# Performance work log

Hardware: AMD Instinct MI355X
Metric: run time of the kernel (lower is better)

The kernel has to match this reference:

```python
import jax, jax.numpy as jnp
import numpy as np

FEAT = 1433
HID = 2
NUM_CLASS = 7
EPS = 1e-5  # torch BatchNorm1d default eps


def _bn_softsign(h, gamma, beta):
    # BatchNorm1d in training mode: batch stats over (batch, length) per channel.
    mu = h.mean(axis=(0, 2), keepdims=True)
    var = h.var(axis=(0, 2), keepdims=True)  # biased, matches torch normalization
    hn = (h - mu) * jax.lax.rsqrt(var + EPS)
    hn = hn * gamma[None, :, None] + beta[None, :, None]
    return hn / (1.0 + jnp.abs(hn))  # Softsign


def feature_adjacency(x, y):
    # (x.unsqueeze(-1) * y.unsqueeze(-2)).sum(dim=1) with x channel dim == 1
    # reduces to an outer product of x[:,0] with neighbor.sum over K.
    adj = jnp.einsum('bf,bg->bfg', x.sum(1), y.sum(1))  # [B,F,F]
    adj = adj + jnp.swapaxes(adj, -1, -2)
    adj = jnp.sqrt(adj)
    # row_normalize: divide by sum over dim 1, zero out inf/nan
    norm = adj / adj.sum(axis=1, keepdims=True)
    norm = jnp.where(jnp.isfinite(norm), norm, 0.0)
    return norm + jnp.eye(FEAT, dtype=x.dtype)


def featbrd(x, adj, W, b):
    # adjacency-based feature conv: y[b,c,f] = sum_g adj[(b),f,g] x[b,c,g],
    # then 1x1 conv over channels (Conv1d kernel_size=1).
    if adj.shape[0] == 1:
        y = jnp.einsum('fg,bcg->bcf', adj[0], x)
    else:
        y = jnp.einsum('bfg,bcg->bcf', adj, x)
    return jnp.einsum('oc,bcf->bof', W, y) + b[None, :, None]


def setup_inputs() -> dict:
    key = jax.random.key(0)
    ks = jax.random.split(key, 10)
    B, K = 64, 8
    inp = {
        'x': jax.random.uniform(ks[0], (B, 1, FEAT), dtype=jnp.float32),
        'neighbor': jax.random.uniform(ks[1], (B, K, FEAT), dtype=jnp.float32),
        'adj_buf': jnp.zeros((1, FEAT, FEAT), jnp.float32),
        'W1': jax.random.normal(ks[2], (HID, 1), jnp.float32) * 0.5,
        'b1': jnp.zeros((HID,), jnp.float32),
        'W2': jax.random.normal(ks[3], (HID, HID), jnp.float32) * 0.5,
        'b2': jnp.zeros((HID,), jnp.float32),
        'g1': jnp.ones((HID,), jnp.float32),
        'be1': jnp.zeros((HID,), jnp.float32),
        'g2': jnp.ones((HID,), jnp.float32),
        'be2': jnp.zeros((HID,), jnp.float32),
        'Wc': jax.random.normal(ks[4], (NUM_CLASS, FEAT * HID), jnp.float32) * 0.02,
        'bc': jnp.zeros((NUM_CLASS,), jnp.float32),
    }
    return inp


def reference(x, neighbor, adj_buf, W1, b1, W2, b2, g1, be1, g2, be2, Wc, bc):
    fadj = feature_adjacency(x, neighbor)          # [B,F,F]
    adj_tot = adj_buf + fadj.sum(0)                # [1,F,F] (buffer starts at zero)
    h = _bn_softsign(featbrd(x, fadj, W1, b1), g1, be1)      # [B,HID,F]
    h = _bn_softsign(featbrd(h, adj_tot, W2, b2), g2, be2)   # [B,HID,F]
    flat = h.reshape(h.shape[0], -1)               # Flatten (C then F, row-major)
    return flat @ Wc.T + bc
```

## Files before the change

### kernel.cpp

```cpp
#include <hip/hip_runtime.h>
#include <hip/hip_bf16.h>
#include <math.h>

constexpr int F   = 1433;
constexpr int NB  = 64;
constexpr int KN  = 8;
constexpr int BF  = NB * F;
constexpr float EPS = 1e-5f;

constexpr int SF  = 16;
constexpr int CH  = (F + SF - 1) / SF;
constexpr int AbS = 1440;
constexpr int SK  = 15;
constexpr int KCH = 96;
constexpr int FT  = 16;
constexpr int NAB = 540;
constexpr int NST = 256;

constexpr int O_YS  = 0;
constexpr int O_DP  = O_YS + BF;
constexpr int O_Y1P = O_DP + SF * BF;
constexpr int O_P   = O_Y1P + SF * BF;
constexpr int O_Y1  = O_P + 4 * BF;
constexpr int O_Y2  = O_Y1 + BF;
constexpr int O_G2P = O_Y2 + 2 * BF;
constexpr int O_AB  = O_G2P + SK * 128 * F;
constexpr int O_ST  = O_AB + (F * AbS) / 2;

__global__ __launch_bounds__(256) void k_D(const float* __restrict__ x,
                                           const float* __restrict__ nbr,
                                           float* __restrict__ DP,
                                           float* __restrict__ ys_out) {
  __shared__ __align__(16) float2 xy[F];
  const int b = blockIdx.x, s = blockIdx.y;
  for (int i = threadIdx.x; i < F; i += 256) {
    const float* p = nbr + (size_t)b * KN * F + i;
    float acc = 0.f;
#pragma unroll
    for (int k = 0; k < KN; ++k) acc += p[k * F];
    xy[i] = make_float2(x[b * F + i], acc);
  }
  __syncthreads();
  if (s == 0) {
    for (int i = threadIdx.x; i < F; i += 256) ys_out[b * F + i] = xy[i].y;
  }
  const int cs = s * CH, cn = min(CH, F - cs);
  float gx[6], gy[6], acc[6] = {};
#pragma unroll
  for (int j = 0; j < 6; ++j) {
    int g = threadIdx.x + 256 * j;
    float2 p = (g < F) ? xy[g] : make_float2(0.f, 0.f);
    gx[j] = p.x; gy[j] = p.y;
  }
#pragma unroll 8
  for (int i = 0; i < cn; ++i) {
    float2 p = xy[cs + i];
#pragma unroll
    for (int j = 0; j < 6; ++j)
      acc[j] += __builtin_amdgcn_sqrtf(fmaf(gy[j], p.x, gx[j] * p.y));
  }
#pragma unroll
  for (int j = 0; j < 6; ++j) {
    int g = threadIdx.x + 256 * j;
    if (g < F) DP[(size_t)s * BF + b * F + g] = acc[j];
  }
}

__global__ __launch_bounds__(256) void k_y1(const float* __restrict__ x,
                                            const float* __restrict__ ys,
                                            const float* __restrict__ DP,
                                            float* __restrict__ Y1P,
                                            float4* __restrict__ P) {
  __shared__ __align__(16) float4 pl[CH];
  const int b = blockIdx.x, s = blockIdx.y;
  const int cs = s * CH, cn = min(CH, F - cs);
  for (int i = threadIdx.x; i < cn; i += 256) {
    int g = cs + i;
    float d = 0.f;
#pragma unroll
    for (int t = 0; t < SF; ++t) d += DP[(size_t)t * BF + b * F + g];
    float inv = (d > 0.f) ? 1.f / d : 0.f;
    float xv = x[b * F + g], yv = ys[b * F + g];
    float4 pv = make_float4(xv, yv, xv * inv, inv);
    pl[i] = pv;
    P[b * F + g] = pv;
  }
  __syncthreads();
  float fx[6], fy[6], acc[6] = {};
#pragma unroll
  for (int j = 0; j < 6; ++j) {
    int f = threadIdx.x + 256 * j;
    fx[j] = (f < F) ? x[b * F + f] : 0.f;
    fy[j] = (f < F) ? ys[b * F + f] : 0.f;
  }
#pragma unroll 8
  for (int i = 0; i < cn; ++i) {
    float4 p = pl[i];
#pragma unroll
    for (int j = 0; j < 6; ++j)
      acc[j] = fmaf(__builtin_amdgcn_sqrtf(fmaf(fx[j], p.y, fy[j] * p.x)), p.z, acc[j]);
  }
#pragma unroll
  for (int j = 0; j < 6; ++j) {
    int f = threadIdx.x + 256 * j;
    if (f < F) Y1P[(size_t)s * BF + b * F + f] = acc[j];
  }
}

__global__ __launch_bounds__(256) void k_Astats(const float* __restrict__ x,
                                                const float* __restrict__ ys,
                                                const float4* __restrict__ P,
                                                const float* __restrict__ Y1P,
                                                __hip_bfloat16* __restrict__ Ab,
                                                float* __restrict__ y1,
                                                float* __restrict__ st) {
  const int bid = blockIdx.x;
  if (bid < NAB) {
    __shared__ float2 fxy[FT][NB];
    const int gx = bid % 6, fy = bid / 6;
    const int fbase = fy * FT;
    for (int i = threadIdx.x; i < FT * NB; i += 256) {
      int b = i >> 4, j = i & 15;
      int f = fbase + j;
      float vx = 0.f, vy = 0.f;
      if (f < F) { vx = x[b * F + f]; vy = ys[b * F + f]; }
      fxy[j][b] = make_float2(vx, vy);
    }
    __syncthreads();
    const int g = gx * 256 + threadIdx.x;
    if (g >= AbS) return;
    if (g < F) {
      float acc[FT] = {};
#pragma unroll 2
      for (int b = 0; b < NB; ++b) {
        float4 p = P[b * F + g];
#pragma unroll
        for (int j = 0; j < FT; ++j) {
          float2 w = fxy[j][b];
          acc[j] = fmaf(__builtin_amdgcn_sqrtf(fmaf(w.x, p.y, p.x * w.y)), p.w, acc[j]);
        }
      }
#pragma unroll
      for (int j = 0; j < FT; ++j) {
        int f = fbase + j;
        if (f < F) Ab[(size_t)f * AbS + g] = __float2bfloat16(acc[j]);
      }
    } else {
#pragma unroll
      for (int j = 0; j < FT; ++j) {
        int f = fbase + j;
        if (f < F) Ab[(size_t)f * AbS + g] = __float2bfloat16(0.f);
      }
    }
  } else {
    const int sid = bid - NAB;
    float s = 0.f, sq = 0.f;
    for (int i = sid * 256 + threadIdx.x; i < BF; i += NST * 256) {
      float v = x[i];
#pragma unroll
      for (int k = 0; k < SF; ++k) v += Y1P[(size_t)k * BF + i];
      y1[i] = v;
      s += v; sq += v * v;
    }
#pragma unroll
    for (int o = 32; o; o >>= 1) {
      s += __shfl_down(s, o, 64);
      sq += __shfl_down(sq, o, 64);
    }
    __shared__ float ls[4], lq[4];
    int wave = threadIdx.x >> 6, lane = threadIdx.x & 63;
    if (lane == 0) { ls[wave] = s; lq[wave] = sq; }
    __syncthreads();
    if (threadIdx.x == 0) {
      atomicAdd(&st[0], ls[0] + ls[1] + ls[2] + ls[3]);
      atomicAdd(&st[1], lq[0] + lq[1] + lq[2] + lq[3]);
    }
  }
}

__global__ __launch_bounds__(256) void k_gemm(const ushort* __restrict__ Ab,
                                              const float* __restrict__ y1,
                                              const float* __restrict__ st,
                                              const float* __restrict__ W1,
                                              const float* __restrict__ g1,
                                              const float* __restrict__ be1,
                                              float* __restrict__ G2P) {
  const float mu = st[0] / (float)BF;
  const float var = st[1] / (float)BF - mu * mu;
  const float wa = W1[0], wb = W1[1];
  const float k0 = wa * g1[0] / sqrtf(wa * wa * var + EPS);
  const float k1 = wb * g1[1] / sqrtf(wb * wb * var + EPS);
  const float c0 = -k0 * mu + be1[0];
  const float c1 = -k1 * mu + be1[1];

  __shared__ __align__(16) float Al[32 * 36];
  __shared__ __align__(16) float Hl[32 * 132];
  const int f0 = blockIdx.x * 32;
  const int gs = blockIdx.y * KCH;
  const int tid = threadIdx.x;
  const int ffs = tid >> 3;
  const int g4s = (tid & 7) * 4;
  const int hb = tid & 7;
  const int hg = tid >> 3;
  const int fsub = (tid & 7) * 4;
  const int msub = (tid >> 3) * 4;
  float acc[4][4] = {};

  for (int c = 0; c < 3; ++c) {
    const int gb = gs + c * 32;
    {
      const int f = f0 + ffs;
      uint2 av = make_uint2(0u, 0u);
      if (f < F) av = *(const uint2*)&Ab[(size_t)f * AbS + gb + g4s];
      Al[(g4s + 0) * 36 + ffs] = __uint_as_float(av.x << 16);
      Al[(g4s + 1) * 36 + ffs] = __uint_as_float(av.x & 0xffff0000u);
      Al[(g4s + 2) * 36 + ffs] = __uint_as_float(av.y << 16);
      Al[(g4s + 3) * 36 + ffs] = __uint_as_float(av.y & 0xffff0000u);
    }
#pragma unroll
    for (int r = 0; r < 8; ++r) {
      const int b = hb + 8 * r;
      const int gl = min(gb + hg, F - 1);
      const float v = y1[b * F + gl];
      float h0 = fmaf(k0, v, c0); h0 = h0 / (1.f + fabsf(h0));
      float h1 = fmaf(k1, v, c1); h1 = h1 / (1.f + fabsf(h1));
      *(float2*)&Hl[hg * 132 + 2 * b] = make_float2(h0, h1);
    }
    __syncthreads();
#pragma unroll 4
    for (int gi = 0; gi < 32; ++gi) {
      float4 a4 = *(const float4*)&Al[gi * 36 + fsub];
      float4 h4 = *(const float4*)&Hl[gi * 132 + msub];
      float av[4] = {a4.x, a4.y, a4.z, a4.w};
      float hv[4] = {h4.x, h4.y, h4.z, h4.w};
#pragma unroll
      for (int i = 0; i < 4; ++i)
#pragma unroll
        for (int j = 0; j < 4; ++j)
          acc[i][j] = fmaf(av[i], hv[j], acc[i][j]);
    }
    __syncthreads();
  }

  float* dst = G2P + (size_t)blockIdx.y * 128 * F;
#pragma unroll
  for (int i = 0; i < 4; ++i) {
    int f = f0 + fsub + i;
    if (f < F) {
#pragma unroll
      for (int j = 0; j < 4; ++j)
        dst[(msub + j) * F + f] = acc[i][j];
    }
  }
}

__global__ __launch_bounds__(256) void k_stats2(const float* __restrict__ y1,
                                                const float* __restrict__ G2P,
                                                const float* __restrict__ st,
                                                const float* __restrict__ W1,
                                                const float* __restrict__ g1,
                                                const float* __restrict__ be1,
                                                float* __restrict__ y2,
                                                float* __restrict__ stw) {
  const float mu = st[0] / (float)BF;
  const float var = st[1] / (float)BF - mu * mu;
  const float wa = W1[0], wb = W1[1];
  const float k0 = wa * g1[0] / sqrtf(wa * wa * var + EPS);
  const float k1 = wb * g1[1] / sqrtf(wb * wb * var + EPS);
  const float c0 = -k0 * mu + be1[0];
  const float c1 = -k1 * mu + be1[1];

  float su = 0.f, sv = 0.f, suu = 0.f, svv = 0.f, suv = 0.f;
  for (int i = blockIdx.x * 256 + threadIdx.x; i < BF; i += gridDim.x * 256) {
    int b = i / F, f = i - b * F;
    float w = y1[i];
    float h0 = fmaf(k0, w, c0); h0 = h0 / (1.f + fabsf(h0));
    float h1 = fmaf(k1, w, c1); h1 = h1 / (1.f + fabsf(h1));
    int iu = (2 * b) * F + f, iv = iu + F;
    float u = 64.f * h0, v = 64.f * h1;
#pragma unroll
    for (int s = 0; s < SK; ++s) {
      u += G2P[(size_t)s * 128 * F + iu];
      v += G2P[(size_t)s * 128 * F + iv];
    }
    y2[iu] = u; y2[iv] = v;
    su += u; sv += v; suu += u * u; svv += v * v; suv += u * v;
  }
#pragma unroll
  for (int o = 32; o; o >>= 1) {
    su += __shfl_down(su, o, 64);
    sv += __shfl_down(sv, o, 64);
    suu += __shfl_down(suu, o, 64);
    svv += __shfl_down(svv, o, 64);
    suv += __shfl_down(suv, o, 64);
  }
  __shared__ float red[5][4];
  int wave = threadIdx.x >> 6, lane = threadIdx.x & 63;
  if (lane == 0) {
    red[0][wave] = su; red[1][wave] = sv; red[2][wave] = suu;
    red[3][wave] = svv; red[4][wave] = suv;
  }
  __syncthreads();
  if (threadIdx.x == 0) {
    atomicAdd(&stw[2], red[0][0] + red[0][1] + red[0][2] + red[0][3]);
    atomicAdd(&stw[3], red[1][0] + red[1][1] + red[1][2] + red[1][3]);
    atomicAdd(&stw[4], red[2][0] + red[2][1] + red[2][2] + red[2][3]);
    atomicAdd(&stw[5], red[3][0] + red[3][1] + red[3][2] + red[3][3]);
    atomicAdd(&stw[6], red[4][0] + red[4][1] + red[4][2] + red[4][3]);
  }
}

__global__ __launch_bounds__(256) void k_out(const float* __restrict__ y2,
                                             const float* __restrict__ st,
                                             const float* __restrict__ W2,
                                             const float* __restrict__ b2,
                                             const float* __restrict__ g2,
                                             const float* __restrict__ be2,
                                             const float* __restrict__ Wc,
                                             const float* __restrict__ bc,
                                             float* __restrict__ out) {
  float n = (float)BF;
  float Eu = st[2] / n, Ev = st[3] / n;
  float Euu = st[4] / n, Evv = st[5] / n, Euv = st[6] / n;
  float cA[2], cB[2], cC[2];
#pragma unroll
  for (int o = 0; o < 2; ++o) {
    float w0 = W2[o * 2 + 0], w1 = W2[o * 2 + 1];
    float mean = w0 * Eu + w1 * Ev + b2[o];
    float Eh2 = w0 * w0 * Euu + 2.f * w0 * w1 * Euv + w1 * w1 * Evv +
                2.f * b2[o] * (w0 * Eu + w1 * Ev) + b2[o] * b2[o];
    float var = Eh2 - mean * mean;
    float inv = g2[o] / sqrtf(var + EPS);
    cA[o] = w0 * inv;
    cB[o] = w1 * inv;
    cC[o] = (b2[o] - mean) * inv + be2[o];
  }
  const int b = blockIdx.x;
  float acc[7] = {};
  for (int f = threadIdx.x; f < F; f += 256) {
    float u = y2[(2 * b) * F + f], v = y2[(2 * b + 1) * F + f];
    float h0 = fmaf(cA[0], u, fmaf(cB[0], v, cC[0]));
    h0 = h0 / (1.f + fabsf(h0));
    float h1 = fmaf(cA[1], u, fmaf(cB[1], v, cC[1]));
    h1 = h1 / (1.f + fabsf(h1));
#pragma unroll
    for (int o = 0; o < 7; ++o) acc[o] = fmaf(Wc[o * (2 * F) + f], h0, acc[o]);
#pragma unroll
    for (int o = 0; o < 7; ++o) acc[o] = fmaf(Wc[o * (2 * F) + F + f], h1, acc[o]);
  }
#pragma unroll
  for (int o = 0; o < 7; ++o) {
#pragma unroll
    for (int s = 32; s; s >>= 1) acc[o] += __shfl_down(acc[o], s, 64);
  }
  __shared__ float red[7][4];
  int wave = threadIdx.x >> 6, lane = threadIdx.x & 63;
  if (lane == 0) {
#pragma unroll
    for (int o = 0; o < 7; ++o) red[o][wave] = acc[o];
  }
  __syncthreads();
  if (threadIdx.x < 7) {
    int o = threadIdx.x;
    out[b * 7 + o] = red[o][0] + red[o][1] + red[o][2] + red[o][3] + bc[o];
  }
}

extern "C" void kernel_launch(void* const* d_in, const int* in_sizes, int n_in,
                              void* d_out, int out_size, void* d_ws, size_t ws_size,
                              hipStream_t stream) {
  const float* x    = (const float*)d_in[0];
  const float* nbr  = (const float*)d_in[1];
  const float* W1   = (const float*)d_in[3];
  const float* W2   = (const float*)d_in[5];
  const float* b2   = (const float*)d_in[6];
  const float* g1   = (const float*)d_in[7];
  const float* be1  = (const float*)d_in[8];
  const float* g2   = (const float*)d_in[9];
  const float* be2  = (const float*)d_in[10];
  const float* Wc   = (const float*)d_in[11];
  const float* bc   = (const float*)d_in[12];
  float* out = (float*)d_out;
  float* ws = (float*)d_ws;

  float*  ys  = ws + O_YS;
  float*  DP  = ws + O_DP;
  float*  Y1P = ws + O_Y1P;
  float4* P   = (float4*)(ws + O_P);
  float*  y1  = ws + O_Y1;
  float*  y2  = ws + O_Y2;
  float*  G2P = ws + O_G2P;
  __hip_bfloat16* Ab = (__hip_bfloat16*)(ws + O_AB);
  float*  st  = ws + O_ST;

  hipMemsetAsync(st, 0, 64 * sizeof(float), stream);

  k_D     <<<dim3(NB, SF), 256, 0, stream>>>(x, nbr, DP, ys);
  k_y1    <<<dim3(NB, SF), 256, 0, stream>>>(x, ys, DP, Y1P, P);
  k_Astats<<<NAB + NST, 256, 0, stream>>>(x, ys, P, Y1P, Ab, y1, st);
  k_gemm  <<<dim3(45, SK), 256, 0, stream>>>((const ushort*)Ab, y1, st, W1, g1, be1, G2P);
  k_stats2<<<NST, 256, 0, stream>>>(y1, G2P, st, W1, g1, be1, y2, st);
  k_out   <<<NB, 256, 0, stream>>>(y2, st, W2, b2, g2, be2, Wc, bc, out);
}
```

Before: 217.6 us.

## Double-buffer GEMM tiles, prefetch P rows, and retune split and tile sizes

The GEMM kernel now uses double-buffered shared-memory tiles and loads the next chunk's A and y1 values into registers while computing on the current one, so global-load latency overlaps with FMAs. The adjacency-build kernel prefetches the next batch row of P. The feature split SF doubles to 32, FT halves to 8 (so twice as many Ab blocks), and the unroll factors change to 5. These changes add shared memory and register pressure, and the larger split increases DP/Y1P partial-sum traffic and memory footprint.

```diff
diff --git a/kernel.cpp b/kernel.cpp
--- a/kernel.cpp
+++ b/kernel.cpp
@@ -8,13 +8,13 @@
 constexpr int BF  = NB * F;
 constexpr float EPS = 1e-5f;
 
-constexpr int SF  = 16;
+constexpr int SF  = 32;
 constexpr int CH  = (F + SF - 1) / SF;
 constexpr int AbS = 1440;
 constexpr int SK  = 15;
 constexpr int KCH = 96;
-constexpr int FT  = 16;
-constexpr int NAB = 540;
+constexpr int FT  = 8;
+constexpr int NAB = 6 * 180;
 constexpr int NST = 256;
 
 constexpr int O_YS  = 0;
@@ -52,7 +52,7 @@
     float2 p = (g < F) ? xy[g] : make_float2(0.f, 0.f);
     gx[j] = p.x; gy[j] = p.y;
   }
-#pragma unroll 8
+#pragma unroll 5
   for (int i = 0; i < cn; ++i) {
     float2 p = xy[cs + i];
 #pragma unroll
@@ -93,7 +93,7 @@
     fx[j] = (f < F) ? x[b * F + f] : 0.f;
     fy[j] = (f < F) ? ys[b * F + f] : 0.f;
   }
-#pragma unroll 8
+#pragma unroll 5
   for (int i = 0; i < cn; ++i) {
     float4 p = pl[i];
 #pragma unroll
@@ -120,7 +120,7 @@
     const int gx = bid % 6, fy = bid / 6;
     const int fbase = fy * FT;
     for (int i = threadIdx.x; i < FT * NB; i += 256) {
-      int b = i >> 4, j = i & 15;
+      int b = i >> 3, j = i & 7;
       int f = fbase + j;
       float vx = 0.f, vy = 0.f;
       if (f < F) { vx = x[b * F + f]; vy = ys[b * F + f]; }
@@ -131,14 +131,17 @@
     if (g >= AbS) return;
     if (g < F) {
       float acc[FT] = {};
+      float4 pc = P[g];
 #pragma unroll 2
       for (int b = 0; b < NB; ++b) {
-        float4 p = P[b * F + g];
+        float4 pn;
+        if (b < NB - 1) pn = P[(b + 1) * F + g];
 #pragma unroll
         for (int j = 0; j < FT; ++j) {
           float2 w = fxy[j][b];
-          acc[j] = fmaf(__builtin_amdgcn_sqrtf(fmaf(w.x, p.y, p.x * w.y)), p.w, acc[j]);
+          acc[j] = fmaf(__builtin_amdgcn_sqrtf(fmaf(w.x, pc.y, pc.x * w.y)), pc.w, acc[j]);
         }
+        pc = pn;
       }
 #pragma unroll
       for (int j = 0; j < FT; ++j) {
@@ -177,6 +180,8 @@
     }
   }
 }
+
+struct GP { uint2 a; float yv[8]; };
 
 __global__ __launch_bounds__(256) void k_gemm(const ushort* __restrict__ Ab,
                                               const float* __restrict__ y1,
@@ -193,8 +198,8 @@
   const float c0 = -k0 * mu + be1[0];
   const float c1 = -k1 * mu + be1[1];
 
-  __shared__ __align__(16) float Al[32 * 36];
-  __shared__ __align__(16) float Hl[32 * 132];
+  __shared__ __align__(16) float Al[2][32 * 36];
+  __shared__ __align__(16) float Hl[2][32 * 132];
   const int f0 = blockIdx.x * 32;
   const int gs = blockIdx.y * KCH;
   const int tid = threadIdx.x;
@@ -204,33 +209,46 @@
   const int hg = tid >> 3;
   const int fsub = (tid & 7) * 4;
   const int msub = (tid >> 3) * 4;
-  float acc[4][4] = {};
-
-  for (int c = 0; c < 3; ++c) {
-    const int gb = gs + c * 32;
-    {
-      const int f = f0 + ffs;
-      uint2 av = make_uint2(0u, 0u);
-      if (f < F) av = *(const uint2*)&Ab[(size_t)f * AbS + gb + g4s];
-      Al[(g4s + 0) * 36 + ffs] = __uint_as_float(av.x << 16);
-      Al[(g4s + 1) * 36 + ffs] = __uint_as_float(av.x & 0xffff0000u);
-      Al[(g4s + 2) * 36 + ffs] = __uint_as_float(av.y << 16);
-      Al[(g4s + 3) * 36 + ffs] = __uint_as_float(av.y & 0xffff0000u);
-    }
+
+  auto loadRegs = [&](int gb, GP& p) {
+    const int f = f0 + ffs;
+    p.a = make_uint2(0u, 0u);
+    if (f < F) p.a = *(const uint2*)&Ab[(size_t)f * AbS + gb + g4s];
+    const int gl = min(gb + hg, F - 1);
+#pragma unroll
+    for (int r = 0; r < 8; ++r) p.yv[r] = y1[(hb + 8 * r) * F + gl];
+  };
+  auto storeLDS = [&](int buf, const GP& p) {
+    Al[buf][(g4s + 0) * 36 + ffs] = __uint_as_float(p.a.x << 16);
+    Al[buf][(g4s + 1) * 36 + ffs] = __uint_as_float(p.a.x & 0xffff0000u);
+    Al[buf][(g4s + 2) * 36 + ffs] = __uint_as_float(p.a.y << 16);
+    Al[buf][(g4s + 3) * 36 + ffs] = __uint_as_float(p.a.y & 0xffff0000u);
 #pragma unroll
     for (int r = 0; r < 8; ++r) {
       const int b = hb + 8 * r;
-      const int gl = min(gb + hg, F - 1);
-      const float v = y1[b * F + gl];
+      const float v = p.yv[r];
       float h0 = fmaf(k0, v, c0); h0 = h0 / (1.f + fabsf(h0));
       float h1 = fmaf(k1, v, c1); h1 = h1 / (1.f + fabsf(h1));
-      *(float2*)&Hl[hg * 132 + 2 * b] = make_float2(h0, h1);
-    }
-    __syncthreads();
+      *(float2*)&Hl[buf][hg * 132 + 2 * b] = make_float2(h0, h1);
+    }
+  };
+
+  float acc[4][4] = {};
+  GP p;
+  loadRegs(gs, p);
+  storeLDS(0, p);
+  __syncthreads();
+
+  for (int c = 0; c < 3; ++c) {
+    const int buf = c & 1;
+    GP pn;
+    if (c < 2) loadRegs(gs + (c + 1) * 32, pn);
+    const float* Ab_ = Al[buf];
+    const float* Hb_ = Hl[buf];
 #pragma unroll 4
     for (int gi = 0; gi < 32; ++gi) {
-      float4 a4 = *(const float4*)&Al[gi * 36 + fsub];
-      float4 h4 = *(const float4*)&Hl[gi * 132 + msub];
+      float4 a4 = *(const float4*)&Ab_[gi * 36 + fsub];
+      float4 h4 = *(const float4*)&Hb_[gi * 132 + msub];
       float av[4] = {a4.x, a4.y, a4.z, a4.w};
       float hv[4] = {h4.x, h4.y, h4.z, h4.w};
 #pragma unroll
@@ -239,6 +257,7 @@
         for (int j = 0; j < 4; ++j)
           acc[i][j] = fmaf(av[i], hv[j], acc[i][j]);
     }
+    if (c < 2) storeLDS(buf ^ 1, pn);
     __syncthreads();
   }
 
```

After: 209.5 us. -3.7%, faster.

## Fuse all stages into one cooperative persistent kernel with grid syncs

Applied to the files above, without the earlier changes.

Replaces the six separate kernel launches and the memset with a single cooperative kernel. It loops over work units per stage and separates stages with grid-wide syncs. The split factors are retuned (SF to 12, FT to 12), and the GEMM stage gains register double-buffering of its next tile loads. The intent is to remove launch gaps and tail idle time between stages, at the cost of grid.sync overhead, a block count capped by occupancy, and an occupancy query on the host every call.

```diff
diff --git a/kernel.cpp b/kernel.cpp
--- a/kernel.cpp
+++ b/kernel.cpp
@@ -1,6 +1,9 @@
 #include <hip/hip_runtime.h>
 #include <hip/hip_bf16.h>
+#include <hip/hip_cooperative_groups.h>
 #include <math.h>
+
+namespace cg = cooperative_groups;
 
 constexpr int F   = 1433;
 constexpr int NB  = 64;
@@ -8,14 +11,13 @@
 constexpr int BF  = NB * F;
 constexpr float EPS = 1e-5f;
 
-constexpr int SF  = 16;
-constexpr int CH  = (F + SF - 1) / SF;
+constexpr int NBLK_MAX = 768;
+constexpr int SF  = 12;
+constexpr int CH  = 120;
 constexpr int AbS = 1440;
 constexpr int SK  = 15;
-constexpr int KCH = 96;
-constexpr int FT  = 16;
-constexpr int NAB = 540;
-constexpr int NST = 256;
+constexpr int FT  = 12;
+constexpr int NA  = 720;
 
 constexpr int O_YS  = 0;
 constexpr int O_DP  = O_YS + BF;
@@ -27,165 +29,179 @@
 constexpr int O_AB  = O_G2P + SK * 128 * F;
 constexpr int O_ST  = O_AB + (F * AbS) / 2;
 
-__global__ __launch_bounds__(256) void k_D(const float* __restrict__ x,
-                                           const float* __restrict__ nbr,
-                                           float* __restrict__ DP,
-                                           float* __restrict__ ys_out) {
-  __shared__ __align__(16) float2 xy[F];
-  const int b = blockIdx.x, s = blockIdx.y;
-  for (int i = threadIdx.x; i < F; i += 256) {
-    const float* p = nbr + (size_t)b * KN * F + i;
-    float acc = 0.f;
-#pragma unroll
-    for (int k = 0; k < KN; ++k) acc += p[k * F];
-    xy[i] = make_float2(x[b * F + i], acc);
-  }
-  __syncthreads();
-  if (s == 0) {
-    for (int i = threadIdx.x; i < F; i += 256) ys_out[b * F + i] = xy[i].y;
-  }
-  const int cs = s * CH, cn = min(CH, F - cs);
-  float gx[6], gy[6], acc[6] = {};
-#pragma unroll
-  for (int j = 0; j < 6; ++j) {
-    int g = threadIdx.x + 256 * j;
-    float2 p = (g < F) ? xy[g] : make_float2(0.f, 0.f);
-    gx[j] = p.x; gy[j] = p.y;
-  }
+__global__ __launch_bounds__(256, 3) void k_mega(
+    const float* __restrict__ x, const float* __restrict__ nbr,
+    const float* __restrict__ W1, const float* __restrict__ g1,
+    const float* __restrict__ be1, const float* __restrict__ W2,
+    const float* __restrict__ b2, const float* __restrict__ g2,
+    const float* __restrict__ be2, const float* __restrict__ Wc,
+    const float* __restrict__ bc, float* __restrict__ out,
+    float* __restrict__ ws) {
+  __shared__ __align__(16) char smem[21504];
+  cg::grid_group grid = cg::this_grid();
+  const int bid = blockIdx.x, tid = threadIdx.x;
+  const int nb = gridDim.x;
+
+  float*  ys  = ws + O_YS;
+  float*  DP  = ws + O_DP;
+  float*  Y1P = ws + O_Y1P;
+  float4* P   = (float4*)(ws + O_P);
+  float*  y1  = ws + O_Y1;
+  float*  y2  = ws + O_Y2;
+  float*  G2P = ws + O_G2P;
+  __hip_bfloat16* Ab = (__hip_bfloat16*)(ws + O_AB);
+  float*  st  = ws + O_ST;
+
+  if (bid == 0 && tid < 64) st[tid] = 0.f;
+
+  for (int u = bid; u < NB * SF; u += nb) {
+    const int b = u & 63, s = u >> 6;
+    const int cs = s * CH, cn = min(CH, F - cs);
+    float2* xy = (float2*)smem;
+    __syncthreads();
+    for (int i = tid; i < F; i += 256) {
+      const float* p = nbr + (size_t)b * KN * F + i;
+      float a = 0.f;
+#pragma unroll
+      for (int k = 0; k < KN; ++k) a += p[k * F];
+      xy[i] = make_float2(x[b * F + i], a);
+    }
+    __syncthreads();
+    if (s == 0)
+      for (int i = tid; i < F; i += 256) ys[b * F + i] = xy[i].y;
+    float gx[6], gy[6], acc[6] = {};
+#pragma unroll
+    for (int j = 0; j < 6; ++j) {
+      int g = tid + 256 * j;
+      float2 p = (g < F) ? xy[g] : make_float2(0.f, 0.f);
+      gx[j] = p.x; gy[j] = p.y;
+    }
 #pragma unroll 8
-  for (int i = 0; i < cn; ++i) {
-    float2 p = xy[cs + i];
-#pragma unroll
-    for (int j = 0; j < 6; ++j)
-      acc[j] += __builtin_amdgcn_sqrtf(fmaf(gy[j], p.x, gx[j] * p.y));
-  }
-#pragma unroll
-  for (int j = 0; j < 6; ++j) {
-    int g = threadIdx.x + 256 * j;
-    if (g < F) DP[(size_t)s * BF + b * F + g] = acc[j];
-  }
-}
-
-__global__ __launch_bounds__(256) void k_y1(const float* __restrict__ x,
-                                            const float* __restrict__ ys,
-                                            const float* __restrict__ DP,
-                                            float* __restrict__ Y1P,
-                                            float4* __restrict__ P) {
-  __shared__ __align__(16) float4 pl[CH];
-  const int b = blockIdx.x, s = blockIdx.y;
-  const int cs = s * CH, cn = min(CH, F - cs);
-  for (int i = threadIdx.x; i < cn; i += 256) {
-    int g = cs + i;
-    float d = 0.f;
-#pragma unroll
-    for (int t = 0; t < SF; ++t) d += DP[(size_t)t * BF + b * F + g];
-    float inv = (d > 0.f) ? 1.f / d : 0.f;
-    float xv = x[b * F + g], yv = ys[b * F + g];
-    float4 pv = make_float4(xv, yv, xv * inv, inv);
-    pl[i] = pv;
-    P[b * F + g] = pv;
-  }
-  __syncthreads();
-  float fx[6], fy[6], acc[6] = {};
-#pragma unroll
-  for (int j = 0; j < 6; ++j) {
-    int f = threadIdx.x + 256 * j;
-    fx[j] = (f < F) ? x[b * F + f] : 0.f;
-    fy[j] = (f < F) ? ys[b * F + f] : 0.f;
-  }
+    for (int i = 0; i < cn; ++i) {
+      float2 p = xy[cs + i];
+#pragma unroll
+      for (int j = 0; j < 6; ++j)
+        acc[j] += __builtin_amdgcn_sqrtf(fmaf(gy[j], p.x, gx[j] * p.y));
+    }
+#pragma unroll
+    for (int j = 0; j < 6; ++j) {
+      int g = tid + 256 * j;
+      if (g < F) DP[(size_t)s * BF + b * F + g] = acc[j];
+    }
+  }
+  grid.sync();
+
+  for (int u = bid; u < NB * SF; u += nb) {
+    const int b = u & 63, s = u >> 6;
+    const int cs = s * CH, cn = min(CH, F - cs);
+    float4* pl = (float4*)smem;
+    __syncthreads();
+    for (int i = tid; i < cn; i += 256) {
+      int g = cs + i;
+      float d = 0.f;
+#pragma unroll
+      for (int t = 0; t < SF; ++t) d += DP[(size_t)t * BF + b * F + g];
+      float inv = (d > 0.f) ? 1.f / d : 0.f;
+      float xv = x[b * F + g], yv = ys[b * F + g];
+      float4 pv = make_float4(xv, yv, xv * inv, inv);
+      pl[i] = pv;
+      P[b * F + g] = pv;
+    }
+    __syncthreads();
+    float fx[6], fy[6], acc[6] = {};
+#pragma unroll
+    for (int j = 0; j < 6; ++j) {
+      int f = tid + 256 * j;
+      fx[j] = (f < F) ? x[b * F + f] : 0.f;
+      fy[j] = (f < F) ? ys[b * F + f] : 0.f;
+    }
 #pragma unroll 8
-  for (int i = 0; i < cn; ++i) {
-    float4 p = pl[i];
-#pragma unroll
-    for (int j = 0; j < 6; ++j)
-      acc[j] = fmaf(__builtin_amdgcn_sqrtf(fmaf(fx[j], p.y, fy[j] * p.x)), p.z, acc[j]);
-  }
-#pragma unroll
-  for (int j = 0; j < 6; ++j) {
-    int f = threadIdx.x + 256 * j;
-    if (f < F) Y1P[(size_t)s * BF + b * F + f] = acc[j];
-  }
-}
-
-__global__ __launch_bounds__(256) void k_Astats(const float* __restrict__ x,
-                                                const float* __restrict__ ys,
-                                                const float4* __restrict__ P,
-                                                const float* __restrict__ Y1P,
-                                                __hip_bfloat16* __restrict__ Ab,
-                                                float* __restrict__ y1,
-                                                float* __restrict__ st) {
-  const int bid = blockIdx.x;
-  if (bid < NAB) {
-    __shared__ float2 fxy[FT][NB];
-    const int gx = bid % 6, fy = bid / 6;
+    for (int i = 0; i < cn; ++i) {
+      float4 p = pl[i];
+#pragma unroll
+      for (int j = 0; j < 6; ++j)
+        acc[j] = fmaf(__builtin_amdgcn_sqrtf(fmaf(fx[j], p.y, fy[j] * p.x)), p.z, acc[j]);
+    }
+#pragma unroll
+    for (int j = 0; j < 6; ++j) {
+      int f = tid + 256 * j;
+      if (f < F) Y1P[(size_t)s * BF + b * F + f] = acc[j];
+    }
+  }
+  grid.sync();
+
+  for (int u = bid; u < NA; u += nb) {
+    float2* fxy = (float2*)smem;
+    const int gxc = u % 6, fy = u / 6;
     const int fbase = fy * FT;
-    for (int i = threadIdx.x; i < FT * NB; i += 256) {
-      int b = i >> 4, j = i & 15;
+    __syncthreads();
+#pragma unroll
+    for (int r = 0; r < 3; ++r) {
+      int i = tid + 256 * r;
+      int j = i >> 6, bb = i & 63;
       int f = fbase + j;
       float vx = 0.f, vy = 0.f;
-      if (f < F) { vx = x[b * F + f]; vy = ys[b * F + f]; }
-      fxy[j][b] = make_float2(vx, vy);
-    }
-    __syncthreads();
-    const int g = gx * 256 + threadIdx.x;
-    if (g >= AbS) return;
-    if (g < F) {
-      float acc[FT] = {};
+      if (f < F) { vx = x[bb * F + f]; vy = ys[bb * F + f]; }
+      fxy[j * 64 + bb] = make_float2(vx, vy);
+    }
+    __syncthreads();
+    const int g = gxc * 256 + tid;
+    if (g < AbS) {
+      if (g < F) {
+        float acc[FT] = {};
+        float4 pc = P[g];
 #pragma unroll 2
-      for (int b = 0; b < NB; ++b) {
-        float4 p = P[b * F + g];
+        for (int bb = 0; bb < NB; ++bb) {
+          float4 pn = pc;
+          if (bb < NB - 1) pn = P[(bb + 1) * F + g];
+#pragma unroll
+          for (int j = 0; j < FT; ++j) {
+            float2 w = fxy[j * 64 + bb];
+            acc[j] = fmaf(__builtin_amdgcn_sqrtf(fmaf(w.x, pc.y, pc.x * w.y)), pc.w, acc[j]);
+          }
+          pc = pn;
+        }
 #pragma unroll
         for (int j = 0; j < FT; ++j) {
-          float2 w = fxy[j][b];
-          acc[j] = fmaf(__builtin_amdgcn_sqrtf(fmaf(w.x, p.y, p.x * w.y)), p.w, acc[j]);
+          int f = fbase + j;
+          if (f < F) Ab[(size_t)f * AbS + g] = __float2bfloat16(acc[j]);
         }
-      }
-#pragma unroll
-      for (int j = 0; j < FT; ++j) {
-        int f = fbase + j;
-        if (f < F) Ab[(size_t)f * AbS + g] = __float2bfloat16(acc[j]);
-      }
-    } else {
-#pragma unroll
-      for (int j = 0; j < FT; ++j) {
-        int f = fbase + j;
-        if (f < F) Ab[(size_t)f * AbS + g] = __float2bfloat16(0.f);
-      }
-    }
-  } else {
-    const int sid = bid - NAB;
-    float s = 0.f, sq = 0.f;
-    for (int i = sid * 256 + threadIdx.x; i < BF; i += NST * 256) {
+      } else {
+#pragma unroll
+        for (int j = 0; j < FT; ++j) {
+          int f = fbase + j;
+          if (f < F) Ab[(size_t)f * AbS + g] = __float2bfloat16(0.f);
+        }
+      }
+    }
+  }
+  {
+    float sv = 0.f, sq = 0.f;
+    for (int i = bid * 256 + tid; i < BF; i += nb * 256) {
       float v = x[i];
 #pragma unroll
-      for (int k = 0; k < SF; ++k) v += Y1P[(size_t)k * BF + i];
+      for (int t = 0; t < SF; ++t) v += Y1P[(size_t)t * BF + i];
       y1[i] = v;
-      s += v; sq += v * v;
+      sv += v; sq += v * v;
     }
 #pragma unroll
     for (int o = 32; o; o >>= 1) {
-      s += __shfl_down(s, o, 64);
+      sv += __shfl_down(sv, o, 64);
       sq += __shfl_down(sq, o, 64);
     }
-    __shared__ float ls[4], lq[4];
-    int wave = threadIdx.x >> 6, lane = threadIdx.x & 63;
-    if (lane == 0) { ls[wave] = s; lq[wave] = sq; }
-    __syncthreads();
-    if (threadIdx.x == 0) {
-      atomicAdd(&st[0], ls[0] + ls[1] + ls[2] + ls[3]);
-      atomicAdd(&st[1], lq[0] + lq[1] + lq[2] + lq[3]);
-    }
-  }
-}
-
-__global__ __launch_bounds__(256) void k_gemm(const ushort* __restrict__ Ab,
-                                              const float* __restrict__ y1,
-                                              const float* __restrict__ st,
-                                              const float* __restrict__ W1,
-                                              const float* __restrict__ g1,
-                                              const float* __restrict__ be1,
-                                              float* __restrict__ G2P) {
-  const float mu = st[0] / (float)BF;
+    float* red = (float*)smem;
+    int wave = tid >> 6, lane = tid & 63;
+    __syncthreads();
+    if (lane == 0) { red[wave] = sv; red[4 + wave] = sq; }
+    __syncthreads();
+    if (tid == 0) {
+      atomicAdd(&st[0], red[0] + red[1] + red[2] + red[3]);
+      atomicAdd(&st[1], red[4] + red[5] + red[6] + red[7]);
+    }
+  }
+  grid.sync();
+
+  const float mu  = st[0] / (float)BF;
   const float var = st[1] / (float)BF - mu * mu;
   const float wa = W1[0], wb = W1[1];
   const float k0 = wa * g1[0] / sqrtf(wa * wa * var + EPS);
@@ -193,176 +209,160 @@
   const float c0 = -k0 * mu + be1[0];
   const float c1 = -k1 * mu + be1[1];
 
-  __shared__ __align__(16) float Al[32 * 36];
-  __shared__ __align__(16) float Hl[32 * 132];
-  const int f0 = blockIdx.x * 32;
-  const int gs = blockIdx.y * KCH;
-  const int tid = threadIdx.x;
-  const int ffs = tid >> 3;
-  const int g4s = (tid & 7) * 4;
-  const int hb = tid & 7;
-  const int hg = tid >> 3;
-  const int fsub = (tid & 7) * 4;
-  const int msub = (tid >> 3) * 4;
-  float acc[4][4] = {};
-
-  for (int c = 0; c < 3; ++c) {
-    const int gb = gs + c * 32;
-    {
+  for (int u = bid; u < 45 * SK; u += nb) {
+    float* Al = (float*)smem;
+    float* Hl = (float*)(smem + 4608);
+    const int ft = u / SK, sk = u % SK;
+    const int f0 = ft * 32, gs = sk * 96;
+    const int ffs = tid >> 3, g4s = (tid & 7) * 4;
+    const int hb = tid & 7, hg = tid >> 3;
+    const int fsub = (tid & 7) * 4, msub = (tid >> 3) * 4;
+
+    uint2 pa; float pyv[8];
+    auto loadRegs = [&](int gb) {
       const int f = f0 + ffs;
-      uint2 av = make_uint2(0u, 0u);
-      if (f < F) av = *(const uint2*)&Ab[(size_t)f * AbS + gb + g4s];
-      Al[(g4s + 0) * 36 + ffs] = __uint_as_float(av.x << 16);
-      Al[(g4s + 1) * 36 + ffs] = __uint_as_float(av.x & 0xffff0000u);
-      Al[(g4s + 2) * 36 + ffs] = __uint_as_float(av.y << 16);
-      Al[(g4s + 3) * 36 + ffs] = __uint_as_float(av.y & 0xffff0000u);
-    }
-#pragma unroll
-    for (int r = 0; r < 8; ++r) {
-      const int b = hb + 8 * r;
+      pa = make_uint2(0u, 0u);
+      if (f < F) pa = *(const uint2*)&Ab[(size_t)f * AbS + gb + g4s];
       const int gl = min(gb + hg, F - 1);
-      const float v = y1[b * F + gl];
-      float h0 = fmaf(k0, v, c0); h0 = h0 / (1.f + fabsf(h0));
-      float h1 = fmaf(k1, v, c1); h1 = h1 / (1.f + fabsf(h1));
-      *(float2*)&Hl[hg * 132 + 2 * b] = make_float2(h0, h1);
-    }
-    __syncthreads();
+#pragma unroll
+      for (int r = 0; r < 8; ++r) pyv[r] = y1[(hb + 8 * r) * F + gl];
+    };
+    auto storeLDS = [&]() {
+      Al[(g4s + 0) * 36 + ffs] = __uint_as_float(pa.x << 16);
+      Al[(g4s + 1) * 36 + ffs] = __uint_as_float(pa.x & 0xffff0000u);
+      Al[(g4s + 2) * 36 + ffs] = __uint_as_float(pa.y << 16);
+      Al[(g4s + 3) * 36 + ffs] = __uint_as_float(pa.y & 0xffff0000u);
+#pragma unroll
+      for (int r = 0; r < 8; ++r) {
+        const int bb = hb + 8 * r;
+        const float v = pyv[r];
+        float h0 = fmaf(k0, v, c0); h0 = h0 / (1.f + fabsf(h0));
+        float h1 = fmaf(k1, v, c1); h1 = h1 / (1.f + fabsf(h1));
+        *(float2*)&Hl[hg * 132 + 2 * bb] = make_float2(h0, h1);
+      }
+    };
+
+    float acc[4][4] = {};
+    loadRegs(gs);
+    for (int c = 0; c < 3; ++c) {
+      __syncthreads();
+      storeLDS();
+      __syncthreads();
+      if (c < 2) loadRegs(gs + (c + 1) * 32);
 #pragma unroll 4
-    for (int gi = 0; gi < 32; ++gi) {
-      float4 a4 = *(const float4*)&Al[gi * 36 + fsub];
-      float4 h4 = *(const float4*)&Hl[gi * 132 + msub];
-      float av[4] = {a4.x, a4.y, a4.z, a4.w};
-      float hv[4] = {h4.x, h4.y, h4.z, h4.w};
-#pragma unroll
-      for (int i = 0; i < 4; ++i)
+      for (int gi = 0; gi < 32; ++gi) {
+        float4 a4 = *(const float4*)&Al[gi * 36 + fsub];
+        float4 h4 = *(const float4*)&Hl[gi * 132 + msub];
+        float av[4] = {a4.x, a4.y, a4.z, a4.w};
+        float hv[4] = {h4.x, h4.y, h4.z, h4.w};
+#pragma unroll
+        for (int i = 0; i < 4; ++i)
+#pragma unroll
+          for (int j = 0; j < 4; ++j)
+            acc[i][j] = fmaf(av[i], hv[j], acc[i][j]);
+      }
+    }
+    float* dst = G2P + (size_t)sk * 128 * F;
+#pragma unroll
+    for (int i = 0; i < 4; ++i) {
+      int f = f0 + fsub + i;
+      if (f < F) {
 #pragma unroll
         for (int j = 0; j < 4; ++j)
-          acc[i][j] = fmaf(av[i], hv[j], acc[i][j]);
-    }
-    __syncthreads();
-  }
-
-  float* dst = G2P + (size_t)blockIdx.y * 128 * F;
-#pragma unroll
-  for (int i = 0; i < 4; ++i) {
-    int f = f0 + fsub + i;
-    if (f < F) {
-#pragma unroll
-      for (int j = 0; j < 4; ++j)
-        dst[(msub + j) * F + f] = acc[i][j];
-    }
-  }
-}
-
-__global__ __launch_bounds__(256) void k_stats2(const float* __restrict__ y1,
-                                                const float* __restrict__ G2P,
-                                                const float* __restrict__ st,
-                                                const float* __restrict__ W1,
-                                                const float* __restrict__ g1,
-                                                const float* __restrict__ be1,
-                                                float* __restrict__ y2,
-                                                float* __restrict__ stw) {
-  const float mu = st[0] / (float)BF;
-  const float var = st[1] / (float)BF - mu * mu;
-  const float wa = W1[0], wb = W1[1];
-  const float k0 = wa * g1[0] / sqrtf(wa * wa * var + EPS);
-  const float k1 = wb * g1[1] / sqrtf(wb * wb * var + EPS);
-  const float c0 = -k0 * mu + be1[0];
-  const float c1 = -k1 * mu + be1[1];
-
-  float su = 0.f, sv = 0.f, suu = 0.f, svv = 0.f, suv = 0.f;
-  for (int i = blockIdx.x * 256 + threadIdx.x; i < BF; i += gridDim.x * 256) {
-    int b = i / F, f = i - b * F;
-    float w = y1[i];
-    float h0 = fmaf(k0, w, c0); h0 = h0 / (1.f + fabsf(h0));
-    float h1 = fmaf(k1, w, c1); h1 = h1 / (1.f + fabsf(h1));
-    int iu = (2 * b) * F + f, iv = iu + F;
-    float u = 64.f * h0, v = 64.f * h1;
-#pragma unroll
-    for (int s = 0; s < SK; ++s) {
-      u += G2P[(size_t)s * 128 * F + iu];
-      v += G2P[(size_t)s * 128 * F + iv];
-    }
-    y2[iu] = u; y2[iv] = v;
-    su += u; sv += v; suu += u * u; svv += v * v; suv += u * v;
-  }
-#pragma unroll
-  for (int o = 32; o; o >>= 1) {
-    su += __shfl_down(su, o, 64);
-    sv += __shfl_down(sv, o, 64);
-    suu += __shfl_down(suu, o, 64);
-    svv += __shfl_down(svv, o, 64);
-    suv += __shfl_down(suv, o, 64);
-  }
-  __shared__ float red[5][4];
-  int wave = threadIdx.x >> 6, lane = threadIdx.x & 63;
-  if (lane == 0) {
-    red[0][wave] = su; red[1][wave] = sv; red[2][wave] = suu;
-    red[3][wave] = svv; red[4][wave] = suv;
-  }
-  __syncthreads();
-  if (threadIdx.x == 0) {
-    atomicAdd(&stw[2], red[0][0] + red[0][1] + red[0][2] + red[0][3]);
-    atomicAdd(&stw[3], red[1][0] + red[1][1] + red[1][2] + red[1][3]);
-    atomicAdd(&stw[4], red[2][0] + red[2][1] + red[2][2] + red[2][3]);
-    atomicAdd(&stw[5], red[3][0] + red[3][1] + red[3][2] + red[3][3]);
-    atomicAdd(&stw[6], red[4][0] + red[4][1] + red[4][2] + red[4][3]);
-  }
-}
-
-__global__ __launch_bounds__(256) void k_out(const float* __restrict__ y2,
-                                             const float* __restrict__ st,
-                                             const float* __restrict__ W2,
-                                             const float* __restrict__ b2,
-                                             const float* __restrict__ g2,
-                                             const float* __restrict__ be2,
-                                             const float* __restrict__ Wc,
-                                             const float* __restrict__ bc,
-                                             float* __restrict__ out) {
-  float n = (float)BF;
-  float Eu = st[2] / n, Ev = st[3] / n;
-  float Euu = st[4] / n, Evv = st[5] / n, Euv = st[6] / n;
-  float cA[2], cB[2], cC[2];
-#pragma unroll
-  for (int o = 0; o < 2; ++o) {
-    float w0 = W2[o * 2 + 0], w1 = W2[o * 2 + 1];
-    float mean = w0 * Eu + w1 * Ev + b2[o];
-    float Eh2 = w0 * w0 * Euu + 2.f * w0 * w1 * Euv + w1 * w1 * Evv +
-                2.f * b2[o] * (w0 * Eu + w1 * Ev) + b2[o] * b2[o];
-    float var = Eh2 - mean * mean;
-    float inv = g2[o] / sqrtf(var + EPS);
-    cA[o] = w0 * inv;
-    cB[o] = w1 * inv;
-    cC[o] = (b2[o] - mean) * inv + be2[o];
-  }
-  const int b = blockIdx.x;
-  float acc[7] = {};
-  for (int f = threadIdx.x; f < F; f += 256) {
-    float u = y2[(2 * b) * F + f], v = y2[(2 * b + 1) * F + f];
-    float h0 = fmaf(cA[0], u, fmaf(cB[0], v, cC[0]));
-    h0 = h0 / (1.f + fabsf(h0));
-    float h1 = fmaf(cA[1], u, fmaf(cB[1], v, cC[1]));
-    h1 = h1 / (1.f + fabsf(h1));
-#pragma unroll
-    for (int o = 0; o < 7; ++o) acc[o] = fmaf(Wc[o * (2 * F) + f], h0, acc[o]);
-#pragma unroll
-    for (int o = 0; o < 7; ++o) acc[o] = fmaf(Wc[o * (2 * F) + F + f], h1, acc[o]);
-  }
-#pragma unroll
-  for (int o = 0; o < 7; ++o) {
-#pragma unroll
-    for (int s = 32; s; s >>= 1) acc[o] += __shfl_down(acc[o], s, 64);
-  }
-  __shared__ float red[7][4];
-  int wave = threadIdx.x >> 6, lane = threadIdx.x & 63;
-  if (lane == 0) {
-#pragma unroll
-    for (int o = 0; o < 7; ++o) red[o][wave] = acc[o];
-  }
-  __syncthreads();
-  if (threadIdx.x < 7) {
-    int o = threadIdx.x;
-    out[b * 7 + o] = red[o][0] + red[o][1] + red[o][2] + red[o][3] + bc[o];
+          dst[(msub + j) * F + f] = acc[i][j];
+      }
+    }
+  }
+  grid.sync();
+
+  {
+    float su = 0.f, svm = 0.f, suu = 0.f, svv = 0.f, suv = 0.f;
+    for (int i = bid * 256 + tid; i < BF; i += nb * 256) {
+      int bb = i / F, f = i - bb * F;
+      float w = y1[i];
+      float h0 = fmaf(k0, w, c0); h0 = h0 / (1.f + fabsf(h0));
+      float h1 = fmaf(k1, w, c1); h1 = h1 / (1.f + fabsf(h1));
+      int iu = (2 * bb) * F + f, iv = iu + F;
+      float u = 64.f * h0, v = 64.f * h1;
+#pragma unroll
+      for (int t = 0; t < SK; ++t) {
+        u += G2P[(size_t)t * 128 * F + iu];
+        v += G2P[(size_t)t * 128 * F + iv];
+      }
+      y2[iu] = u; y2[iv] = v;
+      su += u; svm += v; suu += u * u; svv += v * v; suv += u * v;
+    }
+#pragma unroll
+    for (int o = 32; o; o >>= 1) {
+      su += __shfl_down(su, o, 64);
+      svm += __shfl_down(svm, o, 64);
+      suu += __shfl_down(suu, o, 64);
+      svv += __shfl_down(svv, o, 64);
+      suv += __shfl_down(suv, o, 64);
+    }
+    float* red = (float*)smem;
+    int wave = tid >> 6, lane = tid & 63;
+    __syncthreads();
+    if (lane == 0) {
+      red[0 * 4 + wave] = su; red[1 * 4 + wave] = svm; red[2 * 4 + wave] = suu;
+      red[3 * 4 + wave] = svv; red[4 * 4 + wave] = suv;
+    }
+    __syncthreads();
+    if (tid == 0) {
+#pragma unroll
+      for (int m = 0; m < 5; ++m)
+        atomicAdd(&st[2 + m], red[m * 4 + 0] + red[m * 4 + 1] + red[m * 4 + 2] + red[m * 4 + 3]);
+    }
+  }
+  grid.sync();
+
+  for (int u = bid; u < NB; u += nb) {
+    float n = (float)BF;
+    float Eu = st[2] / n, Ev = st[3] / n;
+    float Euu = st[4] / n, Evv = st[5] / n, Euv = st[6] / n;
+    float cA[2], cB[2], cC[2];
+#pragma unroll
+    for (int o = 0; o < 2; ++o) {
+      float w0 = W2[o * 2 + 0], w1 = W2[o * 2 + 1];
+      float mean = w0 * Eu + w1 * Ev + b2[o];
+      float Eh2 = w0 * w0 * Euu + 2.f * w0 * w1 * Euv + w1 * w1 * Evv +
+                  2.f * b2[o] * (w0 * Eu + w1 * Ev) + b2[o] * b2[o];
+      float vr = Eh2 - mean * mean;
+      float inv = g2[o] / sqrtf(vr + EPS);
+      cA[o] = w0 * inv;
+      cB[o] = w1 * inv;
+      cC[o] = (b2[o] - mean) * inv + be2[o];
+    }
+    const int bb = u;
+    float acc[7] = {};
+    for (int f = tid; f < F; f += 256) {
+      float uu = y2[(2 * bb) * F + f], vv = y2[(2 * bb + 1) * F + f];
+      float h0 = fmaf(cA[0], uu, fmaf(cB[0], vv, cC[0]));
+      h0 = h0 / (1.f + fabsf(h0));
+      float h1 = fmaf(cA[1], uu, fmaf(cB[1], vv, cC[1]));
+      h1 = h1 / (1.f + fabsf(h1));
+#pragma unroll
+      for (int o = 0; o < 7; ++o) acc[o] = fmaf(Wc[o * (2 * F) + f], h0, acc[o]);
+#pragma unroll
+      for (int o = 0; o < 7; ++o) acc[o] = fmaf(Wc[o * (2 * F) + F + f], h1, acc[o]);
+    }
+#pragma unroll
+    for (int o = 0; o < 7; ++o) {
+#pragma unroll
+      for (int sd = 32; sd; sd >>= 1) acc[o] += __shfl_down(acc[o], sd, 64);
+    }
+    float* red = (float*)smem;
+    int wave = tid >> 6, lane = tid & 63;
+    __syncthreads();
+    if (lane == 0) {
+#pragma unroll
+      for (int o = 0; o < 7; ++o) red[o * 4 + wave] = acc[o];
+    }
+    __syncthreads();
+    if (tid < 7) {
+      int o = tid;
+      out[bb * 7 + o] = red[o * 4 + 0] + red[o * 4 + 1] + red[o * 4 + 2] + red[o * 4 + 3] + bc[o];
+    }
   }
 }
 
@@ -381,24 +381,17 @@
   const float* Wc   = (const float*)d_in[11];
   const float* bc   = (const float*)d_in[12];
   float* out = (float*)d_out;
-  float* ws = (float*)d_ws;
-
-  float*  ys  = ws + O_YS;
-  float*  DP  = ws + O_DP;
-  float*  Y1P = ws + O_Y1P;
-  float4* P   = (float4*)(ws + O_P);
-  float*  y1  = ws + O_Y1;
-  float*  y2  = ws + O_Y2;
-  float*  G2P = ws + O_G2P;
-  __hip_bfloat16* Ab = (__hip_bfloat16*)(ws + O_AB);
-  float*  st  = ws + O_ST;
-
-  hipMemsetAsync(st, 0, 64 * sizeof(float), stream);
-
-  k_D     <<<dim3(NB, SF), 256, 0, stream>>>(x, nbr, DP, ys);
-  k_y1    <<<dim3(NB, SF), 256, 0, stream>>>(x, ys, DP, Y1P, P);
-  k_Astats<<<NAB + NST, 256, 0, stream>>>(x, ys, P, Y1P, Ab, y1, st);
-  k_gemm  <<<dim3(45, SK), 256, 0, stream>>>((const ushort*)Ab, y1, st, W1, g1, be1, G2P);
-  k_stats2<<<NST, 256, 0, stream>>>(y1, G2P, st, W1, g1, be1, y2, st);
-  k_out   <<<NB, 256, 0, stream>>>(y2, st, W2, b2, g2, be2, Wc, bc, out);
+  float* ws  = (float*)d_ws;
+
+  int perCU = 0;
+  hipError_t e = hipOccupancyMaxActiveBlocksPerMultiprocessor(&perCU, (const void*)k_mega, 256, 0);
+  if (e != hipSuccess || perCU < 1) perCU = 1;
+  int nblk = perCU * 256;
+  if (nblk > NBLK_MAX) nblk = NBLK_MAX;
+
+  void* args[] = {(void*)&x, (void*)&nbr, (void*)&W1, (void*)&g1, (void*)&be1,
+                  (void*)&W2, (void*)&b2, (void*)&g2, (void*)&be2,
+                  (void*)&Wc, (void*)&bc, (void*)&out, (void*)&ws};
+  hipLaunchCooperativeKernel((const void*)k_mega, dim3(nblk), dim3(256),
+                             args, 0, stream);
 }
```

After: 523.2 us. 2.4x slower.
